# Performance work log

Measured on AMD Instinct MI355X. Metric: run time of the kernel, lower is better.

Reference implementation:

```python
import jax, jax.numpy as jnp
import numpy as np

N = 128        # grid size per dimension
H = 1.0        # grid spacing (module init arg h)
NITER = 128    # Jacobi iterations: enough for wavefront to cross the grid
BIG = 1.0e5    # 'infinity' padding value for boundary neighbors
U0_FAR = 1.0e3 # initial value away from source


def _local_solve(ax, ay, az, fh):
    """Upwind local eikonal solver at each cell.
    ax, ay, az: min of the two axis neighbors per cell. fh = f * h.
    """
    a = jnp.sort(jnp.stack([ax, ay, az], axis=0), axis=0)
    a1, a2, a3 = a[0], a[1], a[2]
    # 1D update
    x1 = a1 + fh
    # 2D update: solve (x-a1)^2 + (x-a2)^2 = fh^2
    disc2 = 2.0 * fh * fh - (a1 - a2) ** 2
    x2 = 0.5 * (a1 + a2 + jnp.sqrt(jnp.maximum(disc2, 0.0)))
    # 3D update: solve sum_i (x-ai)^2 = fh^2
    s = a1 + a2 + a3
    q = a1 * a1 + a2 * a2 + a3 * a3
    disc3 = s * s - 3.0 * (q - fh * fh)
    x3 = (s + jnp.sqrt(jnp.maximum(disc3, 0.0))) / 3.0
    return jnp.where(x1 <= a2, x1, jnp.where(x2 <= a3, x2, x3))


def _step(u, fh):
    up = jnp.pad(u, 1, constant_values=BIG)
    ax = jnp.minimum(up[:-2, 1:-1, 1:-1], up[2:, 1:-1, 1:-1])
    ay = jnp.minimum(up[1:-1, :-2, 1:-1], up[1:-1, 2:, 1:-1])
    az = jnp.minimum(up[1:-1, 1:-1, :-2], up[1:-1, 1:-1, 2:])
    x = _local_solve(ax, ay, az, fh)
    return jnp.minimum(u, x)  # monotone Gauss-Seidel/Jacobi update


def _solve(u0, f):
    fh = f * jnp.float32(H)

    def body(u, _):
        return _step(u, fh), None

    u, _ = jax.lax.scan(jax.checkpoint(body), u0, None, length=NITER)
    return u


def setup_inputs() -> dict:
    key = jax.random.key(0)
    kf = jax.random.fold_in(key, 1)
    # slowness field in [0.5, 1.5]
    f = 0.5 + jax.random.uniform(kf, (N, N, N), dtype=jnp.float32)
    # initial travel-time: large everywhere, 0 at source (grid center)
    u0 = jnp.full((N, N, N), U0_FAR, dtype=jnp.float32)
    u0 = u0.at[N // 2, N // 2, N // 2].set(0.0)
    return {"u0": u0, "f": f}


def reference(u0, f):
    return _solve(u0, f)
```

## Files before the change

kernel.cpp:

```cpp
#include <hip/hip_runtime.h>

#define GN    128
#define GBIG  1.0e5f
#define NITER 128

#define PPY     130
#define PITCH_Y 128
#define PITCH_Z (128 * 130)
#define PADDED_TOTAL (130 * 130 * 128)

#define NBY  16
#define NBZ  64
#define NBLK (NBY * NBZ)

typedef float fx4 __attribute__((ext_vector_type(4)));
typedef int   ix4 __attribute__((ext_vector_type(4)));

__global__ __launch_bounds__(256) void eik_init(const float* __restrict__ u0,
                                                const float* __restrict__ f,
                                                float* __restrict__ uA,
                                                float* __restrict__ uB,
                                                float* __restrict__ fP,
                                                int* __restrict__ inbox) {
    const int i = blockIdx.x * 256 + threadIdx.x;
    if (i < NBLK * 16) {
        const int b = i >> 4, d = i & 15;
        const int by = b % NBY, bz = b / NBY;
        int v = 0;
        if ((d == 0 && by == 0) || (d == 1 && by == NBY - 1) ||
            (d == 2 && bz == 0) || (d == 3 && bz == NBZ - 1))
            v = NITER;
        inbox[i] = v;
    }
    if (i >= PADDED_TOTAL) return;
    const int x = i & 127;
    const int r = i >> 7;
    const int y = r % 130;
    const int z = r / 130;
    float uv = GBIG, fv = 0.0f;
    if (y >= 1 && y <= GN && z >= 1 && z <= GN) {
        const int src = ((z - 1) * GN + (y - 1)) * GN + x;
        uv = u0[src];
        fv = f[src];
    }
    uA[i] = uv;
    uB[i] = uv;
    fP[i] = fv;
}

__device__ __forceinline__ float eik_solve(float ax, float ay, float az,
                                           float fh, float uc) {
    const float a1 = fminf(fminf(ax, ay), az);
    const float a3 = fmaxf(fmaxf(ax, ay), az);
    const float a2 = fmaxf(fminf(fmaxf(ax, ay), az), fminf(ax, ay));
    const float x1 = a1 + fh;
    const float d12 = a1 - a2;
    const float disc2 = 2.0f * fh * fh - d12 * d12;
    const float x2 = 0.5f * (a1 + a2 + sqrtf(fmaxf(disc2, 0.0f)));
    const float s = a1 + a2 + a3;
    const float q = a1 * a1 + a2 * a2 + a3 * a3;
    const float disc3 = s * s - 3.0f * (q - fh * fh);
    const float x3 = (s + sqrtf(fmaxf(disc3, 0.0f))) * (1.0f / 3.0f);
    const float xv = (x1 <= a2) ? x1 : ((x2 <= a3) ? x2 : x3);
    return fminf(uc, xv);
}

__device__ __forceinline__ void pub(int* box, int byteOff, int val) {
    asm volatile("global_store_dword %0, %1, %2 sc1"
                 :: "v"(byteOff), "v"(val), "s"(box) : "memory");
}

__global__ __launch_bounds__(256, 4) void eik_persist(float* __restrict__ uA,
                                                      float* __restrict__ uB,
                                                      const float* __restrict__ fP,
                                                      float* __restrict__ out,
                                                      int* __restrict__ inbox) {
    const int lx = threadIdx.x;
    const int ty = threadIdx.y;
    const int by = blockIdx.y;
    const int bz = blockIdx.z;
    const int tid = ty * 32 + lx;
    const int gy  = by * 8 + ty;
    const int gz0 = bz * 2;
    const int x0  = lx * 4;

    const int dxm = (x0 <= 64 && 64 <= x0 + 3) ? 0
                                               : min(abs(x0 - 64), abs(x0 + 3 - 64));
    const int dy = abs(gy - 64);
    const int d0 = dxm + dy + abs(gz0 - 64);
    const int d1 = dxm + dy + abs(gz0 + 1 - 64);
    const int dmin01 = min(d0, d1);

    const int ry0 = by * 8, ry1 = ry0 + 7;
    const int dymin = (ry0 > 64) ? (ry0 - 64) : ((ry1 < 64) ? (64 - ry1) : 0);
    const int dzmin = min(abs(gz0 - 64), abs(gz0 + 1 - 64));
    const int start = max(1, dymin + dzmin);
    const int dYm = abs(ry0 - 64) + dzmin;
    const int dYp = abs(ry1 - 64) + dzmin;
    const int dZm = abs(gz0 - 64) + dymin;
    const int dZp = abs(gz0 + 1 - 64) + dymin;

    const int idx = bz * NBY + by;
    const int inbOff = idx * 64;
    const int pubYp = (idx + 1) * 64 + 0;
    const int pubYm = (idx - 1) * 64 + 4;
    const int pubZp = (idx + NBY) * 64 + 8;
    const int pubZm = (idx - NBY) * 64 + 12;

    if (tid == 0 && start > 1) {
        const int pv = start - 1;
        if (by < NBY - 1) pub(inbox, pubYp, pv);
        if (by > 0)       pub(inbox, pubYm, pv);
        if (bz < NBZ - 1) pub(inbox, pubZp, pv);
        if (bz > 0)       pub(inbox, pubZm, pv);
    }

    const int base0 = ((gz0 + 1) * PPY + (gy + 1)) * PITCH_Y + x0;
    const int base1 = base0 + PITCH_Z;
    const int vo0  = base0 * 4;
    const int vo1  = base1 * 4;
    const int vozm = vo0 - PITCH_Z * 4;
    const int vozp = vo1 + PITCH_Z * 4;

    fx4 c0 = *(const fx4*)(uA + base0);
    fx4 c1 = *(const fx4*)(uA + base1);
    const fx4 f0 = *(const fx4*)(fP + base0);
    const fx4 f1 = *(const fx4*)(fP + base1);

    for (int i = start; i <= NITER; ++i) {
        const int tYm = (dYm <= i) ? i - 1 : -0x40000000;
        const int tYp = (dYp <= i) ? i - 1 : -0x40000000;
        const int tZm = (dZm <= i) ? i - 1 : -0x40000000;
        const int tZp = (dZp <= i) ? i - 1 : -0x40000000;
        for (;;) {
            ix4 v;
            asm volatile("global_load_dwordx4 %0, %1, %2 sc1\n\t"
                         "s_waitcnt vmcnt(0)"
                         : "=&v"(v) : "v"(inbOff), "s"(inbox) : "memory");
            if (v.x >= tYm && v.y >= tYp && v.z >= tZm && v.w >= tZp) break;
            __builtin_amdgcn_s_sleep(1);
        }

        float xm0 = __shfl_up(c0.w, 1);   if (lx == 0)  xm0 = GBIG;
        float xp0 = __shfl_down(c0.x, 1); if (lx == 31) xp0 = GBIG;
        float xm1 = __shfl_up(c1.w, 1);   if (lx == 0)  xm1 = GBIG;
        float xp1 = __shfl_down(c1.x, 1); if (lx == 31) xp1 = GBIG;

        const bool run = (dmin01 <= i);
        fx4 n0, n1;
        if (run) {
            const float* S = (i & 1) ? uA : uB;
            fx4 ym0, yp0, ym1, yp1, zm, zp;
            asm volatile(
                "global_load_dwordx4 %0, %6, %10 offset:-512 sc1\n\t"
                "global_load_dwordx4 %1, %6, %10 offset:512 sc1\n\t"
                "global_load_dwordx4 %2, %7, %10 offset:-512 sc1\n\t"
                "global_load_dwordx4 %3, %7, %10 offset:512 sc1\n\t"
                "global_load_dwordx4 %4, %8, %10 sc1\n\t"
                "global_load_dwordx4 %5, %9, %10 sc1\n\t"
                "s_waitcnt vmcnt(0)"
                : "=&v"(ym0), "=&v"(yp0), "=&v"(ym1), "=&v"(yp1), "=&v"(zm), "=&v"(zp)
                : "v"(vo0), "v"(vo1), "v"(vozm), "v"(vozp), "s"(S)
                : "memory");

            n0.x = eik_solve(fminf(xm0,  c0.y), fminf(ym0.x, yp0.x), fminf(zm.x, c1.x), f0.x, c0.x);
            n0.y = eik_solve(fminf(c0.x, c0.z), fminf(ym0.y, yp0.y), fminf(zm.y, c1.y), f0.y, c0.y);
            n0.z = eik_solve(fminf(c0.y, c0.w), fminf(ym0.z, yp0.z), fminf(zm.z, c1.z), f0.z, c0.z);
            n0.w = eik_solve(fminf(c0.z, xp0),  fminf(ym0.w, yp0.w), fminf(zm.w, c1.w), f0.w, c0.w);
            n1.x = eik_solve(fminf(xm1,  c1.y), fminf(ym1.x, yp1.x), fminf(c0.x, zp.x), f1.x, c1.x);
            n1.y = eik_solve(fminf(c1.x, c1.z), fminf(ym1.y, yp1.y), fminf(c0.y, zp.y), f1.y, c1.y);
            n1.z = eik_solve(fminf(c1.y, c1.w), fminf(ym1.z, yp1.z), fminf(c0.z, zp.z), f1.z, c1.z);
            n1.w = eik_solve(fminf(c1.z, xp1),  fminf(ym1.w, yp1.w), fminf(c0.w, zp.w), f1.w, c1.w);
        }

        if (i < NITER) {
            float* D = (i & 1) ? uB : uA;
            if (run) {
                if (d0 <= i) {
                    c0 = n0;
                    asm volatile("global_store_dwordx4 %0, %1, %2 sc1"
                                 :: "v"(vo0), "v"(c0), "s"(D) : "memory");
                }
                if (d1 <= i) {
                    c1 = n1;
                    asm volatile("global_store_dwordx4 %0, %1, %2 sc1"
                                 :: "v"(vo1), "v"(c1), "s"(D) : "memory");
                }
            }
            asm volatile("s_waitcnt vmcnt(0)" ::: "memory");
            if (tid == 0 && by > 0)         pub(inbox, pubYm, i);
            if (tid == 224 && by < NBY - 1) pub(inbox, pubYp, i);
            __syncthreads();
            if (tid == 0) {
                if (bz > 0)       pub(inbox, pubZm, i);
                if (bz < NBZ - 1) pub(inbox, pubZp, i);
            }
        } else {
            if (run) {
                if (d0 <= i) c0 = n0;
                if (d1 <= i) c1 = n1;
            }
        }
    }

    float* o = out + (gz0 * GN + gy) * GN + x0;
    *(fx4*)o = c0;
    *(fx4*)(o + GN * GN) = c1;
}

__global__ __launch_bounds__(256) void eik_step(const float* __restrict__ uin,
                                                const float* __restrict__ fP,
                                                float* __restrict__ uout,
                                                int iter) {
    const int lx = threadIdx.x;
    const int gy = blockIdx.y * 8 + threadIdx.y;
    const int gz = blockIdx.z;
    const int x0 = 4 * lx;
    const int dxm = (x0 <= 64 && 64 <= x0 + 3)
                        ? 0
                        : min(abs(x0 - 64), abs(x0 + 3 - 64));
    const int d = dxm + abs(gy - 64) + abs(gz - 64);
    if (d > iter) return;

    const int y = gy + 1;
    const int z = gz + 1;
    const int base = (z * PPY + y) * PITCH_Y + x0;

    const float4 c  = *(const float4*)(uin + base);
    float xm_s = uin[base - 1];
    float xp_s = uin[base + 4];
    if (lx == 0)  xm_s = GBIG;
    if (lx == 31) xp_s = GBIG;
    const float4 ym = *(const float4*)(uin + base - PITCH_Y);
    const float4 yp = *(const float4*)(uin + base + PITCH_Y);
    const float4 zm = *(const float4*)(uin + base - PITCH_Z);
    const float4 zp = *(const float4*)(uin + base + PITCH_Z);
    const float4 f4 = *(const float4*)(fP + base);

    float4 res;
    res.x = eik_solve(fminf(xm_s, c.y), fminf(ym.x, yp.x), fminf(zm.x, zp.x), f4.x, c.x);
    res.y = eik_solve(fminf(c.x, c.z), fminf(ym.y, yp.y), fminf(zm.y, zp.y), f4.y, c.y);
    res.z = eik_solve(fminf(c.y, c.w), fminf(ym.z, yp.z), fminf(zm.z, zp.z), f4.z, c.z);
    res.w = eik_solve(fminf(c.z, xp_s), fminf(ym.w, yp.w), fminf(zm.w, zp.w), f4.w, c.w);

    *(float4*)(uout + base) = res;
}

__global__ __launch_bounds__(256) void eik_extract(const float* __restrict__ uf,
                                                   float* __restrict__ out) {
    const int j = blockIdx.x * 256 + threadIdx.x;
    const int x4 = j & 31;
    const int y  = (j >> 5) & 127;
    const int z  = j >> 12;
    const float4 v =
        *(const float4*)(uf + ((z + 1) * PPY + (y + 1)) * PITCH_Y + 4 * x4);
    *(float4*)(out + 4 * j) = v;
}

extern "C" void kernel_launch(void* const* d_in, const int* in_sizes, int n_in,
                              void* d_out, int out_size, void* d_ws, size_t ws_size,
                              hipStream_t stream) {
    const float* u0 = (const float*)d_in[0];
    const float* f  = (const float*)d_in[1];
    float* out = (float*)d_out;

    float* uA = (float*)d_ws;
    float* uB = uA + PADDED_TOTAL;
    float* fP = uB + PADDED_TOTAL;
    int* inbox = (int*)(fP + PADDED_TOTAL);

    {
        const int nb = (PADDED_TOTAL + 255) / 256;
        eik_init<<<nb, 256, 0, stream>>>(u0, f, uA, uB, fP, inbox);
    }

    static int resident_ok = -1;
    if (resident_ok < 0) {
        int maxb = 0;
        hipError_t qe =
            hipOccupancyMaxActiveBlocksPerMultiprocessor(&maxb, eik_persist, 256, 0);
        resident_ok = (qe == hipSuccess && maxb >= 4) ? 1 : 0;
    }

    if (resident_ok) {
        eik_persist<<<dim3(1, NBY, NBZ), dim3(32, 8, 1), 0, stream>>>(uA, uB, fP,
                                                                      out, inbox);
        return;
    }

    const dim3 block(32, 8, 1);
    const dim3 grid(1, 16, 128);
    for (int i = 1; i <= NITER; ++i) {
        const float* in = (i & 1) ? uA : uB;
        float* o        = (i & 1) ? uB : uA;
        eik_step<<<grid, block, 0, stream>>>(in, fP, o, i);
    }
    eik_extract<<<GN * GN * GN / 4 / 256, 256, 0, stream>>>(uA, out);
}
```

Baseline: 727.9 us.

## Remap blocks to XCD-local slabs and skip coherent cache bypass when neighbors share XCC

Block indices are remapped so that consecutive hardware blocks, which are likely spread round-robin across XCDs, form contiguous z-slabs and more neighbors land on the same die. Each block reads its XCC ID and tags its inbox publications with it. When every neighbor that feeds it reports the same XCC, halo loads and stores use sc0 instead of sc1 so they can hit the die-local L2 rather than going system-coherent. This adds tag masking and branching. It depends on the assumed block-to-XCD placement and on whether sc0 gives correct visibility within one XCC.

After: 726.7 us. Within noise of the previous version (-0.2%).

```diff
diff --git a/kernel.cpp b/kernel.cpp
--- a/kernel.cpp
+++ b/kernel.cpp
@@ -25,10 +25,10 @@
     const int i = blockIdx.x * 256 + threadIdx.x;
     if (i < NBLK * 16) {
         const int b = i >> 4, d = i & 15;
-        const int by = b % NBY, bz = b / NBY;
+        const int ly = b & 15, lz = b >> 4;
         int v = 0;
-        if ((d == 0 && by == 0) || (d == 1 && by == NBY - 1) ||
-            (d == 2 && bz == 0) || (d == 3 && bz == NBZ - 1))
+        if ((d == 0 && ly == 0) || (d == 1 && ly == NBY - 1) ||
+            (d == 2 && lz == 0) || (d == 3 && lz == NBZ - 1))
             v = NITER;
         inbox[i] = v;
     }
@@ -69,6 +69,14 @@
     asm volatile("global_store_dword %0, %1, %2 sc1"
                  :: "v"(byteOff), "v"(val), "s"(box) : "memory");
 }
+__device__ __forceinline__ void stF(float* D, int vo, fx4 v) {
+    asm volatile("global_store_dwordx4 %0, %1, %2"
+                 :: "v"(vo), "v"(v), "s"(D) : "memory");
+}
+__device__ __forceinline__ void stS(float* D, int vo, fx4 v) {
+    asm volatile("global_store_dwordx4 %0, %1, %2 sc1"
+                 :: "v"(vo), "v"(v), "s"(D) : "memory");
+}
 
 __global__ __launch_bounds__(256, 4) void eik_persist(float* __restrict__ uA,
                                                       float* __restrict__ uB,
@@ -77,12 +85,21 @@
                                                       int* __restrict__ inbox) {
     const int lx = threadIdx.x;
     const int ty = threadIdx.y;
-    const int by = blockIdx.y;
-    const int bz = blockIdx.z;
     const int tid = ty * 32 + lx;
-    const int gy  = by * 8 + ty;
-    const int gz0 = bz * 2;
+
+    const int lin  = blockIdx.y + 16 * blockIdx.z;
+    const int slab = lin & 7;
+    const int t    = lin >> 3;
+    const int ly   = t & 15;
+    const int lz   = slab * 8 + (t >> 4);
+
+    const int gy  = ly * 8 + ty;
+    const int gz0 = lz * 2;
     const int x0  = lx * 4;
+
+    int myxcc;
+    asm("s_getreg_b32 %0, hwreg(HW_REG_XCC_ID)" : "=s"(myxcc));
+    const int myx1 = (myxcc & 0xf) + 1;
 
     const int dxm = (x0 <= 64 && 64 <= x0 + 3) ? 0
                                                : min(abs(x0 - 64), abs(x0 + 3 - 64));
@@ -91,7 +108,7 @@
     const int d1 = dxm + dy + abs(gz0 + 1 - 64);
     const int dmin01 = min(d0, d1);
 
-    const int ry0 = by * 8, ry1 = ry0 + 7;
+    const int ry0 = ly * 8, ry1 = ry0 + 7;
     const int dymin = (ry0 > 64) ? (ry0 - 64) : ((ry1 < 64) ? (64 - ry1) : 0);
     const int dzmin = min(abs(gz0 - 64), abs(gz0 + 1 - 64));
     const int start = max(1, dymin + dzmin);
@@ -100,7 +117,7 @@
     const int dZm = abs(gz0 - 64) + dymin;
     const int dZp = abs(gz0 + 1 - 64) + dymin;
 
-    const int idx = bz * NBY + by;
+    const int idx = lz * NBY + ly;
     const int inbOff = idx * 64;
     const int pubYp = (idx + 1) * 64 + 0;
     const int pubYm = (idx - 1) * 64 + 4;
@@ -108,11 +125,11 @@
     const int pubZm = (idx - NBY) * 64 + 12;
 
     if (tid == 0 && start > 1) {
-        const int pv = start - 1;
-        if (by < NBY - 1) pub(inbox, pubYp, pv);
-        if (by > 0)       pub(inbox, pubYm, pv);
-        if (bz < NBZ - 1) pub(inbox, pubZp, pv);
-        if (bz > 0)       pub(inbox, pubZm, pv);
+        const int pv = (myx1 << 16) | (start - 1);
+        if (ly < NBY - 1) pub(inbox, pubYp, pv);
+        if (ly > 0)       pub(inbox, pubYm, pv);
+        if (lz < NBZ - 1) pub(inbox, pubZp, pv);
+        if (lz > 0)       pub(inbox, pubZm, pv);
     }
 
     const int base0 = ((gz0 + 1) * PPY + (gy + 1)) * PITCH_Y + x0;
@@ -132,14 +149,20 @@
         const int tYp = (dYp <= i) ? i - 1 : -0x40000000;
         const int tZm = (dZm <= i) ? i - 1 : -0x40000000;
         const int tZp = (dZp <= i) ? i - 1 : -0x40000000;
+        ix4 v;
         for (;;) {
-            ix4 v;
             asm volatile("global_load_dwordx4 %0, %1, %2 sc1\n\t"
                          "s_waitcnt vmcnt(0)"
                          : "=&v"(v) : "v"(inbOff), "s"(inbox) : "memory");
-            if (v.x >= tYm && v.y >= tYp && v.z >= tZm && v.w >= tZp) break;
+            if ((v.x & 0xffff) >= tYm && (v.y & 0xffff) >= tYp &&
+                (v.z & 0xffff) >= tZm && (v.w & 0xffff) >= tZp) break;
             __builtin_amdgcn_s_sleep(1);
         }
+        const bool af =
+            ((ly == 0)       || (v.x >> 16) == myx1) &&
+            ((ly == NBY - 1) || (v.y >> 16) == myx1) &&
+            ((lz == 0)       || (v.z >> 16) == myx1) &&
+            ((lz == NBZ - 1) || (v.w >> 16) == myx1);
 
         float xm0 = __shfl_up(c0.w, 1);   if (lx == 0)  xm0 = GBIG;
         float xp0 = __shfl_down(c0.x, 1); if (lx == 31) xp0 = GBIG;
@@ -151,17 +174,33 @@
         if (run) {
             const float* S = (i & 1) ? uA : uB;
             fx4 ym0, yp0, ym1, yp1, zm, zp;
-            asm volatile(
-                "global_load_dwordx4 %0, %6, %10 offset:-512 sc1\n\t"
-                "global_load_dwordx4 %1, %6, %10 offset:512 sc1\n\t"
-                "global_load_dwordx4 %2, %7, %10 offset:-512 sc1\n\t"
-                "global_load_dwordx4 %3, %7, %10 offset:512 sc1\n\t"
-                "global_load_dwordx4 %4, %8, %10 sc1\n\t"
-                "global_load_dwordx4 %5, %9, %10 sc1\n\t"
-                "s_waitcnt vmcnt(0)"
-                : "=&v"(ym0), "=&v"(yp0), "=&v"(ym1), "=&v"(yp1), "=&v"(zm), "=&v"(zp)
-                : "v"(vo0), "v"(vo1), "v"(vozm), "v"(vozp), "s"(S)
-                : "memory");
+            if (af) {
+                asm volatile(
+                    "global_load_dwordx4 %0, %6, %10 offset:-512 sc0\n\t"
+                    "global_load_dwordx4 %1, %6, %10 offset:512 sc0\n\t"
+                    "global_load_dwordx4 %2, %7, %10 offset:-512 sc0\n\t"
+                    "global_load_dwordx4 %3, %7, %10 offset:512 sc0\n\t"
+                    "global_load_dwordx4 %4, %8, %10 sc0\n\t"
+                    "global_load_dwordx4 %5, %9, %10 sc0\n\t"
+                    "s_waitcnt vmcnt(0)"
+                    : "=&v"(ym0), "=&v"(yp0), "=&v"(ym1), "=&v"(yp1),
+                      "=&v"(zm), "=&v"(zp)
+                    : "v"(vo0), "v"(vo1), "v"(vozm), "v"(vozp), "s"(S)
+                    : "memory");
+            } else {
+                asm volatile(
+                    "global_load_dwordx4 %0, %6, %10 offset:-512 sc1\n\t"
+                    "global_load_dwordx4 %1, %6, %10 offset:512 sc1\n\t"
+                    "global_load_dwordx4 %2, %7, %10 offset:-512 sc1\n\t"
+                    "global_load_dwordx4 %3, %7, %10 offset:512 sc1\n\t"
+                    "global_load_dwordx4 %4, %8, %10 sc1\n\t"
+                    "global_load_dwordx4 %5, %9, %10 sc1\n\t"
+                    "s_waitcnt vmcnt(0)"
+                    : "=&v"(ym0), "=&v"(yp0), "=&v"(ym1), "=&v"(yp1),
+                      "=&v"(zm), "=&v"(zp)
+                    : "v"(vo0), "v"(vo1), "v"(vozm), "v"(vozp), "s"(S)
+                    : "memory");
+            }
 
             n0.x = eik_solve(fminf(xm0,  c0.y), fminf(ym0.x, yp0.x), fminf(zm.x, c1.x), f0.x, c0.x);
             n0.y = eik_solve(fminf(c0.x, c0.z), fminf(ym0.y, yp0.y), fminf(zm.y, c1.y), f0.y, c0.y);
@@ -176,24 +215,22 @@
         if (i < NITER) {
             float* D = (i & 1) ? uB : uA;
             if (run) {
-                if (d0 <= i) {
-                    c0 = n0;
-                    asm volatile("global_store_dwordx4 %0, %1, %2 sc1"
-                                 :: "v"(vo0), "v"(c0), "s"(D) : "memory");
-                }
-                if (d1 <= i) {
-                    c1 = n1;
-                    asm volatile("global_store_dwordx4 %0, %1, %2 sc1"
-                                 :: "v"(vo1), "v"(c1), "s"(D) : "memory");
+                if (af) {
+                    if (d0 <= i) { c0 = n0; stF(D, vo0, c0); }
+                    if (d1 <= i) { c1 = n1; stF(D, vo1, c1); }
+                } else {
+                    if (d0 <= i) { c0 = n0; stS(D, vo0, c0); }
+                    if (d1 <= i) { c1 = n1; stS(D, vo1, c1); }
                 }
             }
             asm volatile("s_waitcnt vmcnt(0)" ::: "memory");
-            if (tid == 0 && by > 0)         pub(inbox, pubYm, i);
-            if (tid == 224 && by < NBY - 1) pub(inbox, pubYp, i);
+            const int pv = (myx1 << 16) | i;
+            if (tid == 0   && ly > 0)       pub(inbox, pubYm, pv);
+            if (tid == 224 && ly < NBY - 1) pub(inbox, pubYp, pv);
             __syncthreads();
             if (tid == 0) {
-                if (bz > 0)       pub(inbox, pubZm, i);
-                if (bz < NBZ - 1) pub(inbox, pubZp, i);
+                if (lz > 0)       pub(inbox, pubZm, pv);
+                if (lz < NBZ - 1) pub(inbox, pubZp, pv);
             }
         } else {
             if (run) {
```

## Make each wavefront an independent tile and drop block-level barrier

Applied to the files above, without the earlier changes.

Each 64-lane wavefront now owns a 2x2 (y,z) tile with its own inbox and publishes to its neighbours directly, so the per-iteration __syncthreads is gone and synchronisation is per-wave instead of per 8x2 block. The y-neighbour row inside the tile comes from a cross-half shuffle (xor 32), which cuts global loads from six to four per iteration. The cost is four times as many inbox entries and publish stores, plus more spin-polling traffic, and finer-grained dependencies may shorten the critical path of the wavefront-style schedule.

After: 731.3 us. No clear change (+0.5%).

```diff
diff --git a/kernel.cpp b/kernel.cpp
--- a/kernel.cpp
+++ b/kernel.cpp
@@ -9,9 +9,9 @@
 #define PITCH_Z (128 * 130)
 #define PADDED_TOTAL (130 * 130 * 128)
 
-#define NBY  16
-#define NBZ  64
-#define NBLK (NBY * NBZ)
+#define NTY  64
+#define NTZ  64
+#define NTILE (NTY * NTZ)
 
 typedef float fx4 __attribute__((ext_vector_type(4)));
 typedef int   ix4 __attribute__((ext_vector_type(4)));
@@ -23,12 +23,12 @@
                                                 float* __restrict__ fP,
                                                 int* __restrict__ inbox) {
     const int i = blockIdx.x * 256 + threadIdx.x;
-    if (i < NBLK * 16) {
-        const int b = i >> 4, d = i & 15;
-        const int by = b % NBY, bz = b / NBY;
+    if (i < NTILE * 16) {
+        const int t = i >> 4, d = i & 15;
+        const int ly = t & 63, lz = t >> 6;
         int v = 0;
-        if ((d == 0 && by == 0) || (d == 1 && by == NBY - 1) ||
-            (d == 2 && bz == 0) || (d == 3 && bz == NBZ - 1))
+        if ((d == 0 && ly == 0) || (d == 1 && ly == NTY - 1) ||
+            (d == 2 && lz == 0) || (d == 3 && lz == NTZ - 1))
             v = NITER;
         inbox[i] = v;
     }
@@ -65,9 +65,13 @@
     return fminf(uc, xv);
 }
 
-__device__ __forceinline__ void pub(int* box, int byteOff, int val) {
-    asm volatile("global_store_dword %0, %1, %2 sc1"
-                 :: "v"(byteOff), "v"(val), "s"(box) : "memory");
+__device__ __forceinline__ void pubp(int* p, int val) {
+    asm volatile("global_store_dword %0, %1, off sc1"
+                 :: "v"(p), "v"(val) : "memory");
+}
+__device__ __forceinline__ void stS(float* p, fx4 v) {
+    asm volatile("global_store_dwordx4 %0, %1, off sc1"
+                 :: "v"(p), "v"(v) : "memory");
 }
 
 __global__ __launch_bounds__(256, 4) void eik_persist(float* __restrict__ uA,
@@ -75,14 +79,18 @@
                                                       const float* __restrict__ fP,
                                                       float* __restrict__ out,
                                                       int* __restrict__ inbox) {
-    const int lx = threadIdx.x;
-    const int ty = threadIdx.y;
-    const int by = blockIdx.y;
-    const int bz = blockIdx.z;
-    const int tid = ty * 32 + lx;
-    const int gy  = by * 8 + ty;
-    const int gz0 = bz * 2;
-    const int x0  = lx * 4;
+    const int tid  = threadIdx.x;
+    const int w    = tid >> 6;
+    const int lane = tid & 63;
+    const int r    = lane >> 5;
+    const int sub  = lane & 31;
+    const int x0   = sub * 4;
+
+    const int ly = blockIdx.y * 2 + (w & 1);
+    const int lz = blockIdx.z * 2 + (w >> 1);
+    const int gy0 = ly * 2;
+    const int gz0 = lz * 2;
+    const int gy  = gy0 + r;
 
     const int dxm = (x0 <= 64 && 64 <= x0 + 3) ? 0
                                                : min(abs(x0 - 64), abs(x0 + 3 - 64));
@@ -91,36 +99,32 @@
     const int d1 = dxm + dy + abs(gz0 + 1 - 64);
     const int dmin01 = min(d0, d1);
 
-    const int ry0 = by * 8, ry1 = ry0 + 7;
-    const int dymin = (ry0 > 64) ? (ry0 - 64) : ((ry1 < 64) ? (64 - ry1) : 0);
-    const int dzmin = min(abs(gz0 - 64), abs(gz0 + 1 - 64));
+    const int dymin = (gy0 > 64) ? (gy0 - 64) : ((gy0 + 1 < 64) ? (64 - (gy0 + 1)) : 0);
+    const int dzmin = (gz0 > 64) ? (gz0 - 64) : ((gz0 + 1 < 64) ? (64 - (gz0 + 1)) : 0);
     const int start = max(1, dymin + dzmin);
-    const int dYm = abs(ry0 - 64) + dzmin;
-    const int dYp = abs(ry1 - 64) + dzmin;
+    const int dYm = abs(gy0 - 64) + dzmin;
+    const int dYp = abs(gy0 + 1 - 64) + dzmin;
     const int dZm = abs(gz0 - 64) + dymin;
     const int dZp = abs(gz0 + 1 - 64) + dymin;
 
-    const int idx = bz * NBY + by;
-    const int inbOff = idx * 64;
-    const int pubYp = (idx + 1) * 64 + 0;
-    const int pubYm = (idx - 1) * 64 + 4;
-    const int pubZp = (idx + NBY) * 64 + 8;
-    const int pubZm = (idx - NBY) * 64 + 12;
-
-    if (tid == 0 && start > 1) {
+    const int idx = lz * NTY + ly;
+    int* inb = inbox + idx * 16;
+    int* pYp = inbox + (idx + 1) * 16 + 0;
+    int* pYm = inbox + (idx - 1) * 16 + 1;
+    int* pZp = inbox + (idx + NTY) * 16 + 2;
+    int* pZm = inbox + (idx - NTY) * 16 + 3;
+
+    if (lane == 0 && start > 1) {
         const int pv = start - 1;
-        if (by < NBY - 1) pub(inbox, pubYp, pv);
-        if (by > 0)       pub(inbox, pubYm, pv);
-        if (bz < NBZ - 1) pub(inbox, pubZp, pv);
-        if (bz > 0)       pub(inbox, pubZm, pv);
+        if (ly < NTY - 1) pubp(pYp, pv);
+        if (ly > 0)       pubp(pYm, pv);
+        if (lz < NTZ - 1) pubp(pZp, pv);
+        if (lz > 0)       pubp(pZm, pv);
     }
 
     const int base0 = ((gz0 + 1) * PPY + (gy + 1)) * PITCH_Y + x0;
     const int base1 = base0 + PITCH_Z;
-    const int vo0  = base0 * 4;
-    const int vo1  = base1 * 4;
-    const int vozm = vo0 - PITCH_Z * 4;
-    const int vozp = vo1 + PITCH_Z * 4;
+    const int rowoff = (r == 0) ? -PITCH_Y : PITCH_Y;
 
     fx4 c0 = *(const fx4*)(uA + base0);
     fx4 c1 = *(const fx4*)(uA + base1);
@@ -132,68 +136,69 @@
         const int tYp = (dYp <= i) ? i - 1 : -0x40000000;
         const int tZm = (dZm <= i) ? i - 1 : -0x40000000;
         const int tZp = (dZp <= i) ? i - 1 : -0x40000000;
+        ix4 v;
         for (;;) {
-            ix4 v;
-            asm volatile("global_load_dwordx4 %0, %1, %2 sc1\n\t"
+            asm volatile("global_load_dwordx4 %0, %1, off sc1\n\t"
                          "s_waitcnt vmcnt(0)"
-                         : "=&v"(v) : "v"(inbOff), "s"(inbox) : "memory");
+                         : "=&v"(v) : "v"(inb) : "memory");
             if (v.x >= tYm && v.y >= tYp && v.z >= tZm && v.w >= tZp) break;
             __builtin_amdgcn_s_sleep(1);
         }
 
-        float xm0 = __shfl_up(c0.w, 1);   if (lx == 0)  xm0 = GBIG;
-        float xp0 = __shfl_down(c0.x, 1); if (lx == 31) xp0 = GBIG;
-        float xm1 = __shfl_up(c1.w, 1);   if (lx == 0)  xm1 = GBIG;
-        float xp1 = __shfl_down(c1.x, 1); if (lx == 31) xp1 = GBIG;
+        fx4 o0, o1;
+        o0.x = __shfl_xor(c0.x, 32); o0.y = __shfl_xor(c0.y, 32);
+        o0.z = __shfl_xor(c0.z, 32); o0.w = __shfl_xor(c0.w, 32);
+        o1.x = __shfl_xor(c1.x, 32); o1.y = __shfl_xor(c1.y, 32);
+        o1.z = __shfl_xor(c1.z, 32); o1.w = __shfl_xor(c1.w, 32);
+
+        float xm0 = __shfl_up(c0.w, 1);   if (sub == 0)  xm0 = GBIG;
+        float xp0 = __shfl_down(c0.x, 1); if (sub == 31) xp0 = GBIG;
+        float xm1 = __shfl_up(c1.w, 1);   if (sub == 0)  xm1 = GBIG;
+        float xp1 = __shfl_down(c1.x, 1); if (sub == 31) xp1 = GBIG;
 
         const bool run = (dmin01 <= i);
         fx4 n0, n1;
         if (run) {
             const float* S = (i & 1) ? uA : uB;
-            fx4 ym0, yp0, ym1, yp1, zm, zp;
+            fx4 yh0, yh1, zm, zp;
             asm volatile(
-                "global_load_dwordx4 %0, %6, %10 offset:-512 sc1\n\t"
-                "global_load_dwordx4 %1, %6, %10 offset:512 sc1\n\t"
-                "global_load_dwordx4 %2, %7, %10 offset:-512 sc1\n\t"
-                "global_load_dwordx4 %3, %7, %10 offset:512 sc1\n\t"
-                "global_load_dwordx4 %4, %8, %10 sc1\n\t"
-                "global_load_dwordx4 %5, %9, %10 sc1\n\t"
+                "global_load_dwordx4 %0, %4, off sc1\n\t"
+                "global_load_dwordx4 %1, %5, off sc1\n\t"
+                "global_load_dwordx4 %2, %6, off sc1\n\t"
+                "global_load_dwordx4 %3, %7, off sc1\n\t"
                 "s_waitcnt vmcnt(0)"
-                : "=&v"(ym0), "=&v"(yp0), "=&v"(ym1), "=&v"(yp1), "=&v"(zm), "=&v"(zp)
-                : "v"(vo0), "v"(vo1), "v"(vozm), "v"(vozp), "s"(S)
+                : "=&v"(yh0), "=&v"(yh1), "=&v"(zm), "=&v"(zp)
+                : "v"(S + base0 + rowoff), "v"(S + base1 + rowoff),
+                  "v"(S + base0 - PITCH_Z), "v"(S + base1 + PITCH_Z)
                 : "memory");
 
-            n0.x = eik_solve(fminf(xm0,  c0.y), fminf(ym0.x, yp0.x), fminf(zm.x, c1.x), f0.x, c0.x);
-            n0.y = eik_solve(fminf(c0.x, c0.z), fminf(ym0.y, yp0.y), fminf(zm.y, c1.y), f0.y, c0.y);
-            n0.z = eik_solve(fminf(c0.y, c0.w), fminf(ym0.z, yp0.z), fminf(zm.z, c1.z), f0.z, c0.z);
-            n0.w = eik_solve(fminf(c0.z, xp0),  fminf(ym0.w, yp0.w), fminf(zm.w, c1.w), f0.w, c0.w);
-            n1.x = eik_solve(fminf(xm1,  c1.y), fminf(ym1.x, yp1.x), fminf(c0.x, zp.x), f1.x, c1.x);
-            n1.y = eik_solve(fminf(c1.x, c1.z), fminf(ym1.y, yp1.y), fminf(c0.y, zp.y), f1.y, c1.y);
-            n1.z = eik_solve(fminf(c1.y, c1.w), fminf(ym1.z, yp1.z), fminf(c0.z, zp.z), f1.z, c1.z);
-            n1.w = eik_solve(fminf(c1.z, xp1),  fminf(ym1.w, yp1.w), fminf(c0.w, zp.w), f1.w, c1.w);
+            const fx4 ya0 = (r == 0) ? yh0 : o0;
+            const fx4 yb0 = (r == 0) ? o0  : yh0;
+            const fx4 ya1 = (r == 0) ? yh1 : o1;
+            const fx4 yb1 = (r == 0) ? o1  : yh1;
+
+            n0.x = eik_solve(fminf(xm0,  c0.y), fminf(ya0.x, yb0.x), fminf(zm.x, c1.x), f0.x, c0.x);
+            n0.y = eik_solve(fminf(c0.x, c0.z), fminf(ya0.y, yb0.y), fminf(zm.y, c1.y), f0.y, c0.y);
+            n0.z = eik_solve(fminf(c0.y, c0.w), fminf(ya0.z, yb0.z), fminf(zm.z, c1.z), f0.z, c0.z);
+            n0.w = eik_solve(fminf(c0.z, xp0),  fminf(ya0.w, yb0.w), fminf(zm.w, c1.w), f0.w, c0.w);
+            n1.x = eik_solve(fminf(xm1,  c1.y), fminf(ya1.x, yb1.x), fminf(c0.x, zp.x), f1.x, c1.x);
+            n1.y = eik_solve(fminf(c1.x, c1.z), fminf(ya1.y, yb1.y), fminf(c0.y, zp.y), f1.y, c1.y);
+            n1.z = eik_solve(fminf(c1.y, c1.w), fminf(ya1.z, yb1.z), fminf(c0.z, zp.z), f1.z, c1.z);
+            n1.w = eik_solve(fminf(c1.z, xp1),  fminf(ya1.w, yb1.w), fminf(c0.w, zp.w), f1.w, c1.w);
         }
 
         if (i < NITER) {
             float* D = (i & 1) ? uB : uA;
             if (run) {
-                if (d0 <= i) {
-                    c0 = n0;
-                    asm volatile("global_store_dwordx4 %0, %1, %2 sc1"
-                                 :: "v"(vo0), "v"(c0), "s"(D) : "memory");
-                }
-                if (d1 <= i) {
-                    c1 = n1;
-                    asm volatile("global_store_dwordx4 %0, %1, %2 sc1"
-                                 :: "v"(vo1), "v"(c1), "s"(D) : "memory");
-                }
+                if (d0 <= i) { c0 = n0; stS(D + base0, c0); }
+                if (d1 <= i) { c1 = n1; stS(D + base1, c1); }
             }
             asm volatile("s_waitcnt vmcnt(0)" ::: "memory");
-            if (tid == 0 && by > 0)         pub(inbox, pubYm, i);
-            if (tid == 224 && by < NBY - 1) pub(inbox, pubYp, i);
-            __syncthreads();
-            if (tid == 0) {
-                if (bz > 0)       pub(inbox, pubZm, i);
-                if (bz < NBZ - 1) pub(inbox, pubZp, i);
+            if (lane == 0) {
+                if (ly > 0)       pubp(pYm, i);
+                if (ly < NTY - 1) pubp(pYp, i);
+                if (lz > 0)       pubp(pZm, i);
+                if (lz < NTZ - 1) pubp(pZp, i);
             }
         } else {
             if (run) {
@@ -283,8 +288,7 @@
     }
 
     if (resident_ok) {
-        eik_persist<<<dim3(1, NBY, NBZ), dim3(32, 8, 1), 0, stream>>>(uA, uB, fP,
-                                                                      out, inbox);
+        eik_persist<<<dim3(1, 32, 32), 256, 0, stream>>>(uA, uB, fP, out, inbox);
         return;
     }
 
```
